# Kernel tuning notes

Hardware: AMD Instinct MI355X
Metric: run time of the kernel (lower is better)

The kernel has to match this reference:

```python
import jax, jax.numpy as jnp
import numpy as np

D_MODEL = 1024
HEADS = 16
D_K = D_MODEL // HEADS
D_FF = 4096
EPS = 1e-6


def setup_inputs() -> dict:
    key = jax.random.key(0)
    ks = jax.random.split(key, 20)
    B, S, D = 8, 1024, D_MODEL
    sc = 1.0 / np.sqrt(D)
    scf = 1.0 / np.sqrt(D_FF)
    inp = {
        "x": jax.random.normal(ks[0], (B, S, D), jnp.float32),
        "mask": jnp.ones((B, 1, 1, S), jnp.int32),
        "wq": jax.random.normal(ks[1], (D, D), jnp.float32) * sc,
        "bq": jnp.zeros((D,), jnp.float32),
        "wk": jax.random.normal(ks[2], (D, D), jnp.float32) * sc,
        "bk": jnp.zeros((D,), jnp.float32),
        "wv": jax.random.normal(ks[3], (D, D), jnp.float32) * sc,
        "bv": jnp.zeros((D,), jnp.float32),
        "wo": jax.random.normal(ks[4], (D, D), jnp.float32) * sc,
        "bo": jnp.zeros((D,), jnp.float32),
        "w1": jax.random.normal(ks[5], (D_FF, D), jnp.float32) * sc,
        "b1": jnp.zeros((D_FF,), jnp.float32),
        "w2": jax.random.normal(ks[6], (D, D_FF), jnp.float32) * scf,
        "b2": jnp.zeros((D,), jnp.float32),
        "g1": jnp.ones((D,), jnp.float32),
        "be1": jnp.zeros((D,), jnp.float32),
        "g2": jnp.ones((D,), jnp.float32),
        "be2": jnp.zeros((D,), jnp.float32),
    }
    return inp


def _layernorm(x, gamma, beta):
    # Faithful to custom LayerNorm: unbiased std (ddof=1), divide by (std+eps)
    mean = jnp.mean(x, axis=-1, keepdims=True)
    std = jnp.std(x, axis=-1, ddof=1, keepdims=True)
    return gamma * (x - mean) / (std + EPS) + beta


def _mha(x, mask, wq, bq, wk, bk, wv, bv, wo, bo):
    B, S, D = x.shape
    q = x @ wq.T + bq
    k = x @ wk.T + bk
    v = x @ wv.T + bv
    # [B,S,D] -> [B,H,S,dk]
    q = q.reshape(B, S, HEADS, D_K).transpose(0, 2, 1, 3)
    k = k.reshape(B, S, HEADS, D_K).transpose(0, 2, 1, 3)
    v = v.reshape(B, S, HEADS, D_K).transpose(0, 2, 1, 3)
    scores = jnp.einsum("bhqd,bhkd->bhqk", q, k) / np.sqrt(D_K).astype(np.float32)
    scores = jnp.where(mask == 0, jnp.float32(-1e9), scores)
    attn = jax.nn.softmax(scores, axis=-1)
    out = jnp.einsum("bhqk,bhkd->bhqd", attn, v)
    out = out.transpose(0, 2, 1, 3).reshape(B, S, D)
    return out @ wo.T + bo


def reference(x, mask, wq, bq, wk, bk, wv, bv, wo, bo, w1, b1, w2, b2, g1, be1, g2, be2):
    # residual 1: x + MHA(LN(x))
    h = _layernorm(x, g1, be1)
    x = x + _mha(h, mask, wq, bq, wk, bk, wv, bv, wo, bo)
    # residual 2: x + FFN(LN(x))
    h = _layernorm(x, g2, be2)
    ff = jax.nn.relu(h @ w1.T + b1) @ w2.T + b2
    return x + ff
```

## Files before the change

kernel.cpp:

```cpp
#include <hip/hip_runtime.h>

typedef __attribute__((ext_vector_type(8))) short short8;
typedef __attribute__((ext_vector_type(4))) short short4_t;
typedef __attribute__((ext_vector_type(4))) float floatx4;
typedef __attribute__((ext_vector_type(16))) float floatx16;

#define NTOK 8192
#define S_ 1024
#define DM 1024

__device__ __forceinline__ unsigned short f2b(float f) {
    union { float f; unsigned u; } v; v.f = f;
    unsigned r = v.u + 0x7FFF + ((v.u >> 16) & 1);
    return (unsigned short)(r >> 16);
}

__device__ __forceinline__ void gl_lds16(const void* g, void* l) {
    __builtin_amdgcn_global_load_lds((const __attribute__((address_space(1))) void*)g,
                                     (__attribute__((address_space(3))) void*)l, 16, 0, 0);
}

__global__ void cvt_f32_bf16(const float* __restrict__ src, unsigned short* __restrict__ dst, int n) {
    int i = (blockIdx.x * blockDim.x + threadIdx.x) * 4;
    if (i >= n) return;
    float4 v = *reinterpret_cast<const float4*>(src + i);
    short4_t o;
    o.x = (short)f2b(v.x); o.y = (short)f2b(v.y);
    o.z = (short)f2b(v.z); o.w = (short)f2b(v.w);
    *reinterpret_cast<short4_t*>(dst + i) = o;
}

__global__ void copy_f32(const float* __restrict__ src, float* __restrict__ dst, int n) {
    int i = (blockIdx.x * blockDim.x + threadIdx.x) * 4;
    if (i >= n) return;
    *reinterpret_cast<float4*>(dst + i) = *reinterpret_cast<const float4*>(src + i);
}

__global__ void mask_to_bias(const int* __restrict__ mask, float* __restrict__ mb,
                             int* __restrict__ flags, int n) {
    int i = blockIdx.x * blockDim.x + threadIdx.x;
    if (i < n) {
        const int m = mask[i];
        mb[i] = (m == 0) ? -1e9f : 0.f;
        if (m == 0) atomicOr(&flags[i >> 6], 1);
    }
}

__global__ __launch_bounds__(256) void ln_kernel(const float* __restrict__ x,
                                                 const float* __restrict__ g,
                                                 const float* __restrict__ be,
                                                 unsigned short* __restrict__ out) {
    const int row = blockIdx.x;
    const int t = threadIdx.x;
    const float4 xv = *reinterpret_cast<const float4*>(x + (size_t)row * DM + t * 4);
    float s = xv.x + xv.y + xv.z + xv.w;
#pragma unroll
    for (int off = 32; off > 0; off >>= 1) s += __shfl_down(s, off);
    __shared__ float red[8];
    const int wid = t >> 6, lane = t & 63;
    if (lane == 0) red[wid] = s;
    __syncthreads();
    const float mean = (red[0] + red[1] + red[2] + red[3]) * (1.f / 1024.f);
    const float dx = xv.x - mean, dy = xv.y - mean, dz = xv.z - mean, dw = xv.w - mean;
    float ss = dx * dx + dy * dy + dz * dz + dw * dw;
#pragma unroll
    for (int off = 32; off > 0; off >>= 1) ss += __shfl_down(ss, off);
    if (lane == 0) red[4 + wid] = ss;
    __syncthreads();
    const float var = (red[4] + red[5] + red[6] + red[7]) * (1.f / 1023.f);
    const float inv = 1.f / (sqrtf(var) + 1e-6f);
    const float4 gv = *reinterpret_cast<const float4*>(g + t * 4);
    const float4 bv = *reinterpret_cast<const float4*>(be + t * 4);
    short4_t o;
    o.x = (short)f2b(gv.x * dx * inv + bv.x);
    o.y = (short)f2b(gv.y * dy * inv + bv.y);
    o.z = (short)f2b(gv.z * dz * inv + bv.z);
    o.w = (short)f2b(gv.w * dw * inv + bv.w);
    *reinterpret_cast<short4_t*>(out + (size_t)row * DM + t * 4) = o;
}

template <int EPI>
__global__ __launch_bounds__(256, 2) void gemm_bt(const unsigned short* __restrict__ A,
                                                  const unsigned short* __restrict__ Bm,
                                                  const float* __restrict__ bias,
                                                  const float* __restrict__ res,
                                                  void* __restrict__ outp,
                                                  int M, int N, int K, int tilesX) {
    __shared__ __align__(16) unsigned short lds[2][2][8192];
    const int t = threadIdx.x;
    const int lane = t & 63, wid = t >> 6;
    const int wr = wid >> 1, wc = wid & 1;

    const int bid = blockIdx.x;
    const int xcd = bid & 7;
    const int lid = bid >> 3;
    const int sid = lid >> 5;
    const int off = lid & 31;
    const int gsid = sid * 8 + xcd;
    const int supercols = tilesX >> 2;
    const int srow = gsid / supercols;
    const int scol = gsid - srow * supercols;
    const int rowBase = (srow * 8 + (off >> 2)) * 128;
    const int colBase = (scol * 4 + (off & 3)) * 128;

    const int NT = K >> 6;
    const int lr31 = lane & 31;
    const int kh = lane >> 5;

    const unsigned short* Ag[4];
    const unsigned short* Bg[4];
#pragma unroll
    for (int j = 0; j < 4; ++j) {
        const int L = j * 256 + t;
        const int r = L >> 3;
        const int c = ((L & 7) ^ (r & 7)) * 8;
        Ag[j] = A + (size_t)(rowBase + r) * K + c;
        Bg[j] = Bm + (size_t)(colBase + r) * K + c;
    }

    floatx16 acc[2][2] = {};

#pragma unroll
    for (int j = 0; j < 4; ++j) gl_lds16(Ag[j], &lds[0][0][j * 2048 + wid * 512]);
#pragma unroll
    for (int j = 0; j < 4; ++j) gl_lds16(Bg[j], &lds[0][1][j * 2048 + wid * 512]);
#pragma unroll
    for (int j = 0; j < 4; ++j) { Ag[j] += 64; Bg[j] += 64; }

    int cur = 0;
    for (int tt = 0; tt < NT; ++tt) {
        if (tt + 1 < NT) {
#pragma unroll
            for (int j = 0; j < 4; ++j)
                gl_lds16(Ag[j], &lds[cur ^ 1][0][j * 2048 + wid * 512]);
#pragma unroll
            for (int j = 0; j < 4; ++j)
                gl_lds16(Bg[j], &lds[cur ^ 1][1][j * 2048 + wid * 512]);
#pragma unroll
            for (int j = 0; j < 4; ++j) { Ag[j] += 64; Bg[j] += 64; }
            asm volatile("s_waitcnt vmcnt(8)" ::: "memory");
        } else {
            asm volatile("s_waitcnt vmcnt(0)" ::: "memory");
        }
        __builtin_amdgcn_s_barrier();
        __builtin_amdgcn_sched_barrier(0);
        const unsigned short* Ab = &lds[cur][0][0];
        const unsigned short* Bb = &lds[cur][1][0];
#pragma unroll
        for (int ks = 0; ks < 4; ++ks) {
            short8 af[2], bfr[2];
#pragma unroll
            for (int mf = 0; mf < 2; ++mf) {
                const int r = wr * 64 + mf * 32 + lr31;
                const int cp = (ks * 2 + kh) ^ (r & 7);
                af[mf] = *reinterpret_cast<const short8*>(&Ab[r * 64 + cp * 8]);
            }
#pragma unroll
            for (int nf = 0; nf < 2; ++nf) {
                const int r = wc * 64 + nf * 32 + lr31;
                const int cp = (ks * 2 + kh) ^ (r & 7);
                bfr[nf] = *reinterpret_cast<const short8*>(&Bb[r * 64 + cp * 8]);
            }
            __builtin_amdgcn_s_setprio(1);
#pragma unroll
            for (int mf = 0; mf < 2; ++mf)
#pragma unroll
                for (int nf = 0; nf < 2; ++nf)
                    acc[mf][nf] = __builtin_amdgcn_mfma_f32_32x32x16_bf16(af[mf], bfr[nf], acc[mf][nf], 0, 0, 0);
            __builtin_amdgcn_s_setprio(0);
        }
        __builtin_amdgcn_sched_barrier(0);
        __builtin_amdgcn_s_barrier();
        cur ^= 1;
    }

    const int rbw = rowBase + wr * 64;
    const int cbw = colBase + wc * 64;
    const int lc31 = lane & 31;
    if (EPI == 4) {
        unsigned short* qh = (unsigned short*)outp;
        const float SC2 = 0.18033688f;
#pragma unroll
        for (int nf = 0; nf < 2; ++nf) {
            const int c = cbw + nf * 32 + lc31;
            const float bn = bias[c];
            const int sect = c >> 10;
            const int hh = (c >> 6) & 15;
            const int dd = c & 63;
            const float scl = (sect == 0) ? SC2 : 1.f;
#pragma unroll
            for (int mf = 0; mf < 2; ++mf) {
#pragma unroll
                for (int rg = 0; rg < 4; ++rg) {
                    const int r0 = rbw + mf * 32 + rg * 8 + 4 * kh;
                    const int bb = r0 >> 10, ss = r0 & 1023;
                    if (sect == 2) {
                        short4_t pk;
#pragma unroll
                        for (int j = 0; j < 4; ++j) pk[j] = (short)f2b(acc[mf][nf][rg * 4 + j] + bn);
                        *reinterpret_cast<short4_t*>(
                            &qh[16777216 + ((size_t)((bb * 16 + hh) * 64 + dd)) * 1024 + ss]) = pk;
                    } else {
                        unsigned short* base = qh + sect * 8388608;
#pragma unroll
                        for (int j = 0; j < 4; ++j)
                            base[((size_t)((bb * 16 + hh) * 1024 + ss + j)) * 64 + dd] =
                                f2b((acc[mf][nf][rg * 4 + j] + bn) * scl);
                    }
                }
            }
        }
        return;
    }
#pragma unroll
    for (int nf = 0; nf < 2; ++nf) {
        const int c = cbw + nf * 32 + lc31;
        const float bn = bias[c];
#pragma unroll
        for (int mf = 0; mf < 2; ++mf) {
#pragma unroll
            for (int rg = 0; rg < 4; ++rg) {
#pragma unroll
                for (int j = 0; j < 4; ++j) {
                    const int r = rbw + mf * 32 + rg * 8 + 4 * kh + j;
                    float v = acc[mf][nf][rg * 4 + j] + bn;
                    if (EPI == 1) v += res[(size_t)r * N + c];
                    if (EPI == 3) v = fmaxf(v, 0.f);
                    if (EPI == 0 || EPI == 1)
                        ((float*)outp)[(size_t)r * N + c] = v;
                    else
                        ((unsigned short*)outp)[(size_t)r * N + c] = f2b(v);
                }
            }
        }
    }
}

__global__ __launch_bounds__(256) void attn_mfma(const unsigned short* __restrict__ Qh,
                                                 const unsigned short* __restrict__ Kh,
                                                 const unsigned short* __restrict__ Vt,
                                                 const float* __restrict__ mbias,
                                                 const int* __restrict__ mflags,
                                                 unsigned short* __restrict__ out) {
    __shared__ __align__(16) unsigned short Kbuf[2][4096];
    __shared__ __align__(16) unsigned short Vbuf[2][4096];
    __shared__ __align__(16) unsigned short Pbuf[4][16][72];
    __shared__ __align__(16) float mk[1024];
    const int t = threadIdx.x;
    const int w = t >> 6, l = t & 63;
    const int g = l >> 4, q16 = l & 15;
    const int x7 = q16 & 7;
    const int bid = blockIdx.x;
    const int swz = (bid & 7) * 256 + (bid >> 3);
    const int bh = swz >> 4, qb = swz & 15;
    const int b = bh >> 4, h = bh & 15;

    const size_t qbase = ((size_t)bh * 1024 + qb * 64 + w * 16 + q16) * 64;
    const short8 qf0 = *reinterpret_cast<const short8*>(Qh + qbase + g * 8);
    const short8 qf1 = *reinterpret_cast<const short8*>(Qh + qbase + 32 + g * 8);

    const int r0 = t >> 3;
    const int c0 = ((t & 7) ^ (r0 & 7)) * 8;
    const unsigned short* Kg = Kh + (size_t)bh * 65536 + r0 * 64 + c0;
    const unsigned short* Vg = Vt + (size_t)bh * 65536 + r0 * 1024 + c0;

#define ATTN_STAGE(bi, kc_)                                                        \
    do {                                                                           \
        gl_lds16(Kg + (kc_) * 4096, &Kbuf[bi][w * 512]);                           \
        gl_lds16(Kg + (kc_) * 4096 + 2048, &Kbuf[bi][2048 + w * 512]);             \
        gl_lds16(Vg + (kc_) * 64, &Vbuf[bi][w * 512]);                             \
        gl_lds16(Vg + (kc_) * 64 + 32768, &Vbuf[bi][2048 + w * 512]);              \
    } while (0)

    gl_lds16(mbias + b * 1024 + t * 4, &mk[w * 256]);
    ATTN_STAGE(0, 0);

    floatx4 oacc[4] = {};
    floatx4 loacc = {};
    short8 ones;
#pragma unroll
    for (int j = 0; j < 8; ++j) ones[j] = (short)0x3F80;

    int cur = 0;
    for (int kc = 0; kc < 16; ++kc) {
        if (kc < 15) {
            ATTN_STAGE(cur ^ 1, kc + 1);
            asm volatile("s_waitcnt vmcnt(4)" ::: "memory");
        } else {
            asm volatile("s_waitcnt vmcnt(0)" ::: "memory");
        }
        __builtin_amdgcn_s_barrier();
        __builtin_amdgcn_sched_barrier(0);
        const unsigned short* Kb = Kbuf[cur];
        const unsigned short* Vb = Vbuf[cur];

        floatx4 st[4] = {};
        __builtin_amdgcn_s_setprio(1);
#pragma unroll
        for (int t4 = 0; t4 < 4; ++t4) {
            const int row = t4 * 16 + q16;
            const short8 kf0 = *reinterpret_cast<const short8*>(&Kb[row * 64 + (g ^ x7) * 8]);
            const short8 kf1 = *reinterpret_cast<const short8*>(&Kb[row * 64 + ((4 + g) ^ x7) * 8]);
            st[t4] = __builtin_amdgcn_mfma_f32_16x16x32_bf16(kf0, qf0, st[t4], 0, 0, 0);
            st[t4] = __builtin_amdgcn_mfma_f32_16x16x32_bf16(kf1, qf1, st[t4], 0, 0, 0);
        }
        __builtin_amdgcn_s_setprio(0);

        if (mflags[b * 16 + kc]) {
#pragma unroll
            for (int t4 = 0; t4 < 4; ++t4) {
                const float4 mbv = *reinterpret_cast<const float4*>(&mk[kc * 64 + t4 * 16 + g * 4]);
#pragma unroll
                for (int r = 0; r < 4; ++r) st[t4][r] += ((const float*)&mbv)[r];
            }
        }
#pragma unroll
        for (int t4 = 0; t4 < 4; ++t4) {
            const float p0 = __builtin_exp2f(st[t4][0]);
            const float p1 = __builtin_exp2f(st[t4][1]);
            const float p2 = __builtin_exp2f(st[t4][2]);
            const float p3 = __builtin_exp2f(st[t4][3]);
            unsigned u0, u1;
            asm("v_cvt_pk_bf16_f32 %0, %1, %2" : "=v"(u0) : "v"(p0), "v"(p1));
            asm("v_cvt_pk_bf16_f32 %0, %1, %2" : "=v"(u1) : "v"(p2), "v"(p3));
            uint2 pr; pr.x = u0; pr.y = u1;
            *reinterpret_cast<uint2*>(&Pbuf[w][q16][t4 * 16 + g * 4]) = pr;
        }

        const short8 pf0 = *reinterpret_cast<const short8*>(&Pbuf[w][q16][g * 8]);
        const short8 pf1 = *reinterpret_cast<const short8*>(&Pbuf[w][q16][32 + g * 8]);
        __builtin_amdgcn_s_setprio(1);
        loacc = __builtin_amdgcn_mfma_f32_16x16x32_bf16(pf0, ones, loacc, 0, 0, 0);
        loacc = __builtin_amdgcn_mfma_f32_16x16x32_bf16(pf1, ones, loacc, 0, 0, 0);
#pragma unroll
        for (int n = 0; n < 4; ++n) {
            const int row = n * 16 + q16;
            const short8 vf0 = *reinterpret_cast<const short8*>(&Vb[row * 64 + (g ^ x7) * 8]);
            const short8 vf1 = *reinterpret_cast<const short8*>(&Vb[row * 64 + ((4 + g) ^ x7) * 8]);
            oacc[n] = __builtin_amdgcn_mfma_f32_16x16x32_bf16(pf0, vf0, oacc[n], 0, 0, 0);
            oacc[n] = __builtin_amdgcn_mfma_f32_16x16x32_bf16(pf1, vf1, oacc[n], 0, 0, 0);
        }
        __builtin_amdgcn_s_setprio(0);
        __builtin_amdgcn_sched_barrier(0);
        __builtin_amdgcn_s_barrier();
        cur ^= 1;
    }
#undef ATTN_STAGE

    const size_t obase = ((size_t)b * S_ + qb * 64 + w * 16) * 1024 + h * 64;
#pragma unroll
    for (int r = 0; r < 4; ++r) {
        const float invr = 1.f / loacc[r];
        const size_t orow = obase + (size_t)(g * 4 + r) * 1024;
#pragma unroll
        for (int n = 0; n < 4; ++n)
            out[orow + n * 16 + q16] = f2b(oacc[n][r] * invr);
    }
}

extern "C" void kernel_launch(void* const* d_in, const int* in_sizes, int n_in,
                              void* d_out, int out_size, void* d_ws, size_t ws_size,
                              hipStream_t stream) {
    const float* x   = (const float*)d_in[0];
    const int*  mask = (const int*)d_in[1];
    const float* wq  = (const float*)d_in[2];
    const float* bq  = (const float*)d_in[3];
    const float* wk  = (const float*)d_in[4];
    const float* bk  = (const float*)d_in[5];
    const float* wv  = (const float*)d_in[6];
    const float* bv  = (const float*)d_in[7];
    const float* wo  = (const float*)d_in[8];
    const float* bo  = (const float*)d_in[9];
    const float* w1  = (const float*)d_in[10];
    const float* b1  = (const float*)d_in[11];
    const float* w2  = (const float*)d_in[12];
    const float* b2  = (const float*)d_in[13];
    const float* g1  = (const float*)d_in[14];
    const float* be1 = (const float*)d_in[15];
    const float* g2  = (const float*)d_in[16];
    const float* be2 = (const float*)d_in[17];

    char* ws = (char*)d_ws;
    unsigned short* wqkv_bf = (unsigned short*)(ws);
    unsigned short* wo_bf   = (unsigned short*)(ws + 6291456);
    unsigned short* w1_bf   = (unsigned short*)(ws + 8388608);
    unsigned short* w2_bf   = (unsigned short*)(ws + 16777216);
    float*          bqkv    = (float*)(ws + 25165824);
    float*          mbias   = (float*)(ws + 25178112);
    int*            mflags  = (int*)(ws + 25210880);
    unsigned short* h_bf    = (unsigned short*)(ws + 25214976);
    float*          x1      = (float*)(ws + 41992192);
    unsigned short* attn_bf = (unsigned short*)(ws + 75546624);
    unsigned short* qkvh    = (unsigned short*)(ws + 92323840);
    unsigned short* ff1_bf  = (unsigned short*)(ws + 92323840);

    cvt_f32_bf16<<<1024, 256, 0, stream>>>(wq, wqkv_bf, 1048576);
    cvt_f32_bf16<<<1024, 256, 0, stream>>>(wk, wqkv_bf + 1048576, 1048576);
    cvt_f32_bf16<<<1024, 256, 0, stream>>>(wv, wqkv_bf + 2097152, 1048576);
    cvt_f32_bf16<<<1024, 256, 0, stream>>>(wo, wo_bf, 1048576);
    cvt_f32_bf16<<<4096, 256, 0, stream>>>(w1, w1_bf, 4194304);
    cvt_f32_bf16<<<4096, 256, 0, stream>>>(w2, w2_bf, 4194304);
    copy_f32<<<1, 256, 0, stream>>>(bq, bqkv, 1024);
    copy_f32<<<1, 256, 0, stream>>>(bk, bqkv + 1024, 1024);
    copy_f32<<<1, 256, 0, stream>>>(bv, bqkv + 2048, 1024);
    hipMemsetAsync(mflags, 0, 128 * sizeof(int), stream);
    mask_to_bias<<<32, 256, 0, stream>>>(mask, mbias, mflags, 8192);

    ln_kernel<<<NTOK, 256, 0, stream>>>(x, g1, be1, h_bf);
    gemm_bt<4><<<24 * 64, 256, 0, stream>>>(h_bf, wqkv_bf, bqkv, nullptr, qkvh, NTOK, 3072, 1024, 24);
    attn_mfma<<<2048, 256, 0, stream>>>(qkvh, qkvh + 8388608, qkvh + 16777216, mbias, mflags, attn_bf);
    gemm_bt<1><<<8 * 64, 256, 0, stream>>>(attn_bf, wo_bf, bo, x, x1, NTOK, 1024, 1024, 8);
    ln_kernel<<<NTOK, 256, 0, stream>>>(x1, g2, be2, h_bf);
    gemm_bt<3><<<32 * 64, 256, 0, stream>>>(h_bf, w1_bf, b1, nullptr, ff1_bf, NTOK, 4096, 1024, 32);
    gemm_bt<1><<<8 * 64, 256, 0, stream>>>(ff1_bf, w2_bf, b2, x1, (float*)d_out, NTOK, 1024, 4096, 8);
}
```

Measured before the change: 382.3 us.

## Add 256x256-tile 8-wave GEMM for QKV and FFN1 projections

Adds a new GEMM kernel with 512 threads per block (8 waves) that computes a 256x256 output tile. It uses double-buffered direct global-to-LDS loads with an XOR-swizzled layout, and 16x16x32 bf16 MFMAs interleaved with staggered stage loads. It replaces the 128x128 gemm_bt for the QKV projection (head-split epilogue) and the FFN1 ReLU GEMM, aiming for more data reuse per LDS load and fewer blocks. The old gemm_bt is reduced to the residual-add fp32 epilogue only. The trade-off is a larger LDS footprint and register pressure, which limits occupancy.

```diff
diff --git a/kernel.cpp b/kernel.cpp
--- a/kernel.cpp
+++ b/kernel.cpp
@@ -80,11 +80,157 @@
 }
 
 template <int EPI>
+__global__ __launch_bounds__(512, 2) void gemm8p(const unsigned short* __restrict__ A,
+                                                 const unsigned short* __restrict__ Bm,
+                                                 const float* __restrict__ bias,
+                                                 void* __restrict__ outp,
+                                                 int M, int N, int K, int tilesX) {
+    __shared__ __align__(16) unsigned short Abuf[2][16384];
+    __shared__ __align__(16) unsigned short Bbuf[2][16384];
+    const int t = threadIdx.x;
+    const int lane = t & 63, wid = t >> 6;
+    const int wr = wid >> 2, wc = wid & 3;
+
+    const int nwg = gridDim.x;
+    const int bid = blockIdx.x;
+    const int swz = (bid & 7) * (nwg >> 3) + (bid >> 3);
+    const int rowBase = (swz / tilesX) * 256;
+    const int colBase = (swz % tilesX) * 256;
+
+    const int NT = K >> 6;
+    const int l15 = lane & 15, l4 = lane >> 4;
+
+    const int tr = t >> 3;
+    const int tc = ((t & 7) ^ (tr & 7)) * 8;
+    const int ldst = tr * 64 + (t & 7) * 8;
+    const unsigned short* As_[2][2];
+    const unsigned short* Bs_[2][2];
+#pragma unroll
+    for (int h = 0; h < 2; ++h)
+#pragma unroll
+        for (int j = 0; j < 2; ++j) {
+            As_[h][j] = A + (size_t)(rowBase + j * 128 + h * 64 + tr) * K + tc;
+            Bs_[h][j] = Bm + (size_t)(colBase + h * 128 + j * 64 + tr) * K + tc;
+        }
+
+#define STG_B(h_, b_, kk_)                                                    \
+    do {                                                                      \
+        gl_lds16(Bs_[h_][0] + (kk_), &Bbuf[b_][(h_)*8192 + ldst]);            \
+        gl_lds16(Bs_[h_][1] + (kk_), &Bbuf[b_][(h_)*8192 + 4096 + ldst]);     \
+    } while (0)
+#define STG_A(h_, b_, kk_)                                                    \
+    do {                                                                      \
+        gl_lds16(As_[h_][0] + (kk_), &Abuf[b_][(h_)*8192 + ldst]);            \
+        gl_lds16(As_[h_][1] + (kk_), &Abuf[b_][(h_)*8192 + 4096 + ldst]);     \
+    } while (0)
+
+    floatx4 acc[8][4] = {};
+
+    STG_B(0, 0, 0); STG_B(1, 0, 0); STG_A(0, 0, 0); STG_A(1, 0, 0);
+
+    for (int kt = 0; kt < NT; ++kt) {
+        const int cur = kt & 1, nxt = cur ^ 1;
+        const int kkn = (kt + 1 < NT ? kt + 1 : kt) << 6;
+        short8 bfr[4][2];
+#pragma unroll
+        for (int q = 0; q < 4; ++q) {
+            if (q == 0) STG_B(0, nxt, kkn);
+            if (q == 1) STG_B(1, nxt, kkn);
+            if (q == 2) STG_A(0, nxt, kkn);
+            if (q == 3) STG_A(1, nxt, kkn);
+            if (q == 0) asm volatile("s_waitcnt vmcnt(4)" ::: "memory");
+            if (q == 2) asm volatile("s_waitcnt vmcnt(6)" ::: "memory");
+            __builtin_amdgcn_s_barrier();
+            __builtin_amdgcn_sched_barrier(0);
+            if (q == 0) {
+#pragma unroll
+                for (int n = 0; n < 4; ++n)
+#pragma unroll
+                    for (int ks = 0; ks < 2; ++ks) {
+                        const int rho = wc * 64 + n * 16 + l15;
+                        const int cp = (l4 + 4 * ks) ^ (rho & 7);
+                        bfr[n][ks] = *reinterpret_cast<const short8*>(&Bbuf[cur][rho * 64 + cp * 8]);
+                    }
+            }
+            short8 af[2][2];
+#pragma unroll
+            for (int m = 0; m < 2; ++m)
+#pragma unroll
+                for (int ks = 0; ks < 2; ++ks) {
+                    const int wlr = q * 32 + m * 16 + l15;
+                    const int rho = ((wlr >> 6) * 2 + wr) * 64 + (wlr & 63);
+                    const int cp = (l4 + 4 * ks) ^ (wlr & 7);
+                    af[m][ks] = *reinterpret_cast<const short8*>(&Abuf[cur][rho * 64 + cp * 8]);
+                }
+            __builtin_amdgcn_s_setprio(1);
+#pragma unroll
+            for (int m = 0; m < 2; ++m)
+#pragma unroll
+                for (int n = 0; n < 4; ++n) {
+                    acc[q * 2 + m][n] = __builtin_amdgcn_mfma_f32_16x16x32_bf16(af[m][0], bfr[n][0], acc[q * 2 + m][n], 0, 0, 0);
+                    acc[q * 2 + m][n] = __builtin_amdgcn_mfma_f32_16x16x32_bf16(af[m][1], bfr[n][1], acc[q * 2 + m][n], 0, 0, 0);
+                }
+            __builtin_amdgcn_s_setprio(0);
+            __builtin_amdgcn_sched_barrier(0);
+        }
+    }
+#undef STG_A
+#undef STG_B
+
+    const int lrow = l4 * 4, lcol = l15;
+    if (EPI == 4) {
+        unsigned short* qh = (unsigned short*)outp;
+        const float SC2 = 0.18033688f;
+#pragma unroll
+        for (int n = 0; n < 4; ++n) {
+            const int c = colBase + wc * 64 + n * 16 + lcol;
+            const float bn = bias[c];
+            const int sect = c >> 10;
+            const int hh = (c >> 6) & 15;
+            const int dd = c & 63;
+            const float scl = (sect == 0) ? SC2 : 1.f;
+#pragma unroll
+            for (int f = 0; f < 8; ++f) {
+                const int r0 = rowBase + wr * 128 + f * 16 + lrow;
+                const int bb = r0 >> 10, ss = r0 & 1023;
+                if (sect == 2) {
+                    short4_t pk;
+#pragma unroll
+                    for (int j = 0; j < 4; ++j) pk[j] = (short)f2b(acc[f][n][j] + bn);
+                    *reinterpret_cast<short4_t*>(
+                        &qh[16777216 + ((size_t)((bb * 16 + hh) * 64 + dd)) * 1024 + ss]) = pk;
+                } else {
+                    unsigned short* base = qh + sect * 8388608;
+#pragma unroll
+                    for (int j = 0; j < 4; ++j)
+                        base[((size_t)((bb * 16 + hh) * 1024 + ss + j)) * 64 + dd] =
+                            f2b((acc[f][n][j] + bn) * scl);
+                }
+            }
+        }
+        return;
+    }
+#pragma unroll
+    for (int n = 0; n < 4; ++n) {
+        const int c = colBase + wc * 64 + n * 16 + lcol;
+        const float bn = bias[c];
+#pragma unroll
+        for (int f = 0; f < 8; ++f) {
+            const int r0 = rowBase + wr * 128 + f * 16 + lrow;
+#pragma unroll
+            for (int j = 0; j < 4; ++j) {
+                float v = fmaxf(acc[f][n][j] + bn, 0.f);
+                ((unsigned short*)outp)[(size_t)(r0 + j) * N + c] = f2b(v);
+            }
+        }
+    }
+}
+
 __global__ __launch_bounds__(256, 2) void gemm_bt(const unsigned short* __restrict__ A,
                                                   const unsigned short* __restrict__ Bm,
                                                   const float* __restrict__ bias,
                                                   const float* __restrict__ res,
-                                                  void* __restrict__ outp,
+                                                  float* __restrict__ outp,
                                                   int M, int N, int K, int tilesX) {
     __shared__ __align__(16) unsigned short lds[2][2][8192];
     const int t = threadIdx.x;
@@ -177,41 +323,6 @@
     const int rbw = rowBase + wr * 64;
     const int cbw = colBase + wc * 64;
     const int lc31 = lane & 31;
-    if (EPI == 4) {
-        unsigned short* qh = (unsigned short*)outp;
-        const float SC2 = 0.18033688f;
-#pragma unroll
-        for (int nf = 0; nf < 2; ++nf) {
-            const int c = cbw + nf * 32 + lc31;
-            const float bn = bias[c];
-            const int sect = c >> 10;
-            const int hh = (c >> 6) & 15;
-            const int dd = c & 63;
-            const float scl = (sect == 0) ? SC2 : 1.f;
-#pragma unroll
-            for (int mf = 0; mf < 2; ++mf) {
-#pragma unroll
-                for (int rg = 0; rg < 4; ++rg) {
-                    const int r0 = rbw + mf * 32 + rg * 8 + 4 * kh;
-                    const int bb = r0 >> 10, ss = r0 & 1023;
-                    if (sect == 2) {
-                        short4_t pk;
-#pragma unroll
-                        for (int j = 0; j < 4; ++j) pk[j] = (short)f2b(acc[mf][nf][rg * 4 + j] + bn);
-                        *reinterpret_cast<short4_t*>(
-                            &qh[16777216 + ((size_t)((bb * 16 + hh) * 64 + dd)) * 1024 + ss]) = pk;
-                    } else {
-                        unsigned short* base = qh + sect * 8388608;
-#pragma unroll
-                        for (int j = 0; j < 4; ++j)
-                            base[((size_t)((bb * 16 + hh) * 1024 + ss + j)) * 64 + dd] =
-                                f2b((acc[mf][nf][rg * 4 + j] + bn) * scl);
-                    }
-                }
-            }
-        }
-        return;
-    }
 #pragma unroll
     for (int nf = 0; nf < 2; ++nf) {
         const int c = cbw + nf * 32 + lc31;
@@ -222,14 +333,8 @@
             for (int rg = 0; rg < 4; ++rg) {
 #pragma unroll
                 for (int j = 0; j < 4; ++j) {
-                    const int r = rbw + mf * 32 + rg * 8 + 4 * kh + j;
-                    float v = acc[mf][nf][rg * 4 + j] + bn;
-                    if (EPI == 1) v += res[(size_t)r * N + c];
-                    if (EPI == 3) v = fmaxf(v, 0.f);
-                    if (EPI == 0 || EPI == 1)
-                        ((float*)outp)[(size_t)r * N + c] = v;
-                    else
-                        ((unsigned short*)outp)[(size_t)r * N + c] = f2b(v);
+                    const int r = rbw + mf * 32 + rg * 8 + 4 * (lane >> 5) + j;
+                    outp[(size_t)r * N + c] = acc[mf][nf][rg * 4 + j] + bn + res[(size_t)r * N + c];
                 }
             }
         }
@@ -407,10 +512,10 @@
     mask_to_bias<<<32, 256, 0, stream>>>(mask, mbias, mflags, 8192);
 
     ln_kernel<<<NTOK, 256, 0, stream>>>(x, g1, be1, h_bf);
-    gemm_bt<4><<<24 * 64, 256, 0, stream>>>(h_bf, wqkv_bf, bqkv, nullptr, qkvh, NTOK, 3072, 1024, 24);
+    gemm8p<4><<<384, 512, 0, stream>>>(h_bf, wqkv_bf, bqkv, qkvh, NTOK, 3072, 1024, 12);
     attn_mfma<<<2048, 256, 0, stream>>>(qkvh, qkvh + 8388608, qkvh + 16777216, mbias, mflags, attn_bf);
-    gemm_bt<1><<<8 * 64, 256, 0, stream>>>(attn_bf, wo_bf, bo, x, x1, NTOK, 1024, 1024, 8);
+    gemm_bt<<<8 * 64, 256, 0, stream>>>(attn_bf, wo_bf, bo, x, x1, NTOK, 1024, 1024, 8);
     ln_kernel<<<NTOK, 256, 0, stream>>>(x1, g2, be2, h_bf);
-    gemm_bt<3><<<32 * 64, 256, 0, stream>>>(h_bf, w1_bf, b1, nullptr, ff1_bf, NTOK, 4096, 1024, 32);
-    gemm_bt<1><<<8 * 64, 256, 0, stream>>>(ff1_bf, w2_bf, b2, x1, (float*)d_out, NTOK, 1024, 4096, 8);
-}
+    gemm8p<3><<<512, 512, 0, stream>>>(h_bf, w1_bf, b1, ff1_bf, NTOK, 4096, 1024, 16);
+    gemm_bt<<<8 * 64, 256, 0, stream>>>(ff1_bf, w2_bf, b2, x1, (float*)d_out, NTOK, 1024, 4096, 8);
+}
```

Result: slower. 395.1 us (+3.3%).

## Add 256x256-tile 512-thread GEMM with XCD-aware swizzle for FFN1

Applied to the files above, without the earlier changes.

Adds a new bf16 MFMA GEMM kernel with 256x256 output tiles, 8 waves, double-buffered LDS filled by direct global-to-LDS loads, XOR-swizzled LDS layout, interleaved fragment reads and MFMA with priority hints, and a block-to-tile mapping grouped per XCD. It replaces the 4096-wide FFN1 GEMM (bias+ReLU, bf16 output). Larger tiles raise arithmetic intensity and L2 reuse, in exchange for fewer blocks and more registers and LDS per block. The generic epilogue is also reduced to the residual-add float path, since the remaining gemm_bt uses appear to be EPI=1 only.

```diff
diff --git a/kernel.cpp b/kernel.cpp
--- a/kernel.cpp
+++ b/kernel.cpp
@@ -223,13 +223,132 @@
 #pragma unroll
                 for (int j = 0; j < 4; ++j) {
                     const int r = rbw + mf * 32 + rg * 8 + 4 * kh + j;
-                    float v = acc[mf][nf][rg * 4 + j] + bn;
-                    if (EPI == 1) v += res[(size_t)r * N + c];
-                    if (EPI == 3) v = fmaxf(v, 0.f);
-                    if (EPI == 0 || EPI == 1)
-                        ((float*)outp)[(size_t)r * N + c] = v;
-                    else
-                        ((unsigned short*)outp)[(size_t)r * N + c] = f2b(v);
+                    ((float*)outp)[(size_t)r * N + c] =
+                        acc[mf][nf][rg * 4 + j] + bn + res[(size_t)r * N + c];
+                }
+            }
+        }
+    }
+}
+
+__global__ __launch_bounds__(512, 2) void gemm256p(const unsigned short* __restrict__ A,
+                                                   const unsigned short* __restrict__ Bm,
+                                                   const float* __restrict__ bias,
+                                                   unsigned short* __restrict__ outp,
+                                                   int M, int N, int K, int tilesX) {
+    __shared__ __align__(16) unsigned short Abuf[2][16384];
+    __shared__ __align__(16) unsigned short Bbuf[2][16384];
+    const int t = threadIdx.x;
+    const int lane = t & 63, wid = t >> 6;
+    const int wr = wid >> 2, wc = wid & 3;
+
+    const int bid = blockIdx.x;
+    const int xcd = bid & 7;
+    const int lid = bid >> 3;
+    const int sid = lid >> 5;
+    const int off = lid & 31;
+    const int gsid = sid * 8 + xcd;
+    const int supercols = tilesX >> 2;
+    const int srow = gsid / supercols;
+    const int scol = gsid - srow * supercols;
+    const int rowBase = (srow * 8 + (off >> 2)) * 256;
+    const int colBase = (scol * 4 + (off & 3)) * 256;
+
+    const int NT = K >> 6;
+    const int lr31 = lane & 31;
+    const int kh = lane >> 5;
+    const int x7 = lane & 7;
+
+    const int tr = t >> 3;
+    const int c0 = ((t & 7) ^ (tr & 7)) * 8;
+    const int ldst = t * 8;
+    const unsigned short* Asrc[4];
+    const unsigned short* Bsrc[4];
+#pragma unroll
+    for (int u = 0; u < 4; ++u) {
+        Asrc[u] = A + (size_t)(rowBase + u * 64 + tr) * K + c0;
+        Bsrc[u] = Bm + (size_t)(colBase + u * 64 + tr) * K + c0;
+    }
+
+#define STG_A(b_, kk_)                                                      \
+    do {                                                                    \
+        _Pragma("unroll") for (int u = 0; u < 4; ++u)                       \
+            gl_lds16(Asrc[u] + (kk_), &Abuf[b_][u * 4096 + ldst]);          \
+    } while (0)
+#define STG_B(b_, kk_)                                                      \
+    do {                                                                    \
+        _Pragma("unroll") for (int u = 0; u < 4; ++u)                       \
+            gl_lds16(Bsrc[u] + (kk_), &Bbuf[b_][u * 4096 + ldst]);          \
+    } while (0)
+#define READQ(q_, af_, bf_)                                                             \
+    do {                                                                                \
+        _Pragma("unroll") for (int mf = 0; mf < 4; ++mf) {                              \
+            const int rho = wr * 128 + mf * 32 + lr31;                                  \
+            (af_)[mf] = *reinterpret_cast<const short8*>(                               \
+                &Abuf[cur][rho * 64 + ((2 * (q_) + kh) ^ x7) * 8]);                     \
+        }                                                                               \
+        _Pragma("unroll") for (int nf = 0; nf < 2; ++nf) {                              \
+            const int rho = wc * 64 + nf * 32 + lr31;                                   \
+            (bf_)[nf] = *reinterpret_cast<const short8*>(                               \
+                &Bbuf[cur][rho * 64 + ((2 * (q_) + kh) ^ x7) * 8]);                     \
+        }                                                                               \
+    } while (0)
+#define MFMAQ(af_, bf_)                                                                 \
+    do {                                                                                \
+        __builtin_amdgcn_s_setprio(1);                                                  \
+        _Pragma("unroll") for (int mf = 0; mf < 4; ++mf)                                \
+            _Pragma("unroll") for (int nf = 0; nf < 2; ++nf)                            \
+                acc[mf][nf] = __builtin_amdgcn_mfma_f32_32x32x16_bf16((af_)[mf],        \
+                                  (bf_)[nf], acc[mf][nf], 0, 0, 0);                     \
+        __builtin_amdgcn_s_setprio(0);                                                  \
+    } while (0)
+
+    floatx16 acc[4][2] = {};
+
+    STG_A(0, 0);
+    STG_B(0, 0);
+
+    short8 afA[4], bfA[2], afB[4], bfB[2];
+    for (int kt = 0; kt < NT; ++kt) {
+        const int cur = kt & 1, nxt = cur ^ 1;
+        const bool pf = (kt + 1 < NT);
+        const int kkn = (pf ? kt + 1 : kt) << 6;
+        __builtin_amdgcn_s_barrier();
+        if (pf) STG_A(nxt, kkn);
+        if (pf) asm volatile("s_waitcnt vmcnt(4)" ::: "memory");
+        else    asm volatile("s_waitcnt vmcnt(0)" ::: "memory");
+        __builtin_amdgcn_sched_barrier(0);
+        READQ(0, afA, bfA);
+        if (pf) STG_B(nxt, kkn);
+        READQ(1, afB, bfB);
+        MFMAQ(afA, bfA);
+        READQ(2, afA, bfA);
+        MFMAQ(afB, bfB);
+        READQ(3, afB, bfB);
+        MFMAQ(afA, bfA);
+        MFMAQ(afB, bfB);
+    }
+#undef STG_A
+#undef STG_B
+#undef READQ
+#undef MFMAQ
+
+    const int rbw = rowBase + wr * 128;
+    const int cbw = colBase + wc * 64;
+    const int lc31 = lane & 31;
+#pragma unroll
+    for (int nf = 0; nf < 2; ++nf) {
+        const int c = cbw + nf * 32 + lc31;
+        const float bn = bias[c];
+#pragma unroll
+        for (int mf = 0; mf < 4; ++mf) {
+#pragma unroll
+            for (int rg = 0; rg < 4; ++rg) {
+                const int r0 = rbw + mf * 32 + rg * 8 + 4 * kh;
+#pragma unroll
+                for (int j = 0; j < 4; ++j) {
+                    const float v = fmaxf(acc[mf][nf][rg * 4 + j] + bn, 0.f);
+                    outp[(size_t)(r0 + j) * N + c] = f2b(v);
                 }
             }
         }
@@ -411,6 +530,6 @@
     attn_mfma<<<2048, 256, 0, stream>>>(qkvh, qkvh + 8388608, qkvh + 16777216, mbias, mflags, attn_bf);
     gemm_bt<1><<<8 * 64, 256, 0, stream>>>(attn_bf, wo_bf, bo, x, x1, NTOK, 1024, 1024, 8);
     ln_kernel<<<NTOK, 256, 0, stream>>>(x1, g2, be2, h_bf);
-    gemm_bt<3><<<32 * 64, 256, 0, stream>>>(h_bf, w1_bf, b1, nullptr, ff1_bf, NTOK, 4096, 1024, 32);
+    gemm256p<<<512, 512, 0, stream>>>(h_bf, w1_bf, b1, ff1_bf, NTOK, 4096, 1024, 16);
     gemm_bt<1><<<8 * 64, 256, 0, stream>>>(ff1_bf, w2_bf, b2, x1, (float*)d_out, NTOK, 1024, 4096, 8);
 }
```

After: 380.2 us. About the same (-0.6%).
